# Performance work log

Measured on AMD Instinct MI355X. Metric: run time of the kernel, lower is better.

Reference implementation:

```python
import jax, jax.numpy as jnp
import numpy as np

K_NEIGHBORS = 3  # init kwarg k_neighbors


def setup_inputs() -> dict:
    key = jax.random.key(0)
    k1, k2 = jax.random.split(key)
    q = jax.random.normal(k1, (75, 640, 21, 21), dtype=jnp.float32)
    S = jax.random.normal(k2, (5, 640, 21, 21), dtype=jnp.float32)
    return {"q": q, "S": S, "qAV_num": 1, "SAV_num": 1, "shot_num": 1}


def reference(q, S, qAV_num, SAV_num, shot_num):
    B, C = q.shape[0], q.shape[1]
    # [B, HW, C], L2-normalize each local descriptor over channels
    qd = q.reshape(B, C, -1).transpose(0, 2, 1)
    qd = qd / jnp.linalg.norm(qd, axis=2, keepdims=True)

    N = S.shape[0]
    sd = S.reshape(N, C, -1).transpose(0, 2, 1)  # [N, HW, C]
    sd = sd / jnp.linalg.norm(sd, axis=2, keepdims=True)
    HW = sd.shape[1]
    M = SAV_num * shot_num * HW
    # group support images into classes: [ncls, C, M]
    sup = sd.reshape(-1, M, C).transpose(0, 2, 1)
    ncls = sup.shape[0]

    # cosine similarity: [B, ncls, HW, M]
    ip = jnp.einsum('bqc,ncm->bnqm', qd, sup)
    # split AV groups: [B//qAV, qAV, ncls, HW, M]
    ip = ip.reshape(B // qAV_num, qAV_num, ncls, HW, M)
    # top-k along the query-descriptor (HW) axis (torch dim=-2)
    topk = jax.lax.top_k(jnp.swapaxes(ip, -1, -2), K_NEIGHBORS)[0]  # [..., M, k]
    img2class = topk.sum(axis=(-1, -2))  # [B', qAV, ncls]
    # geometric mean over the AV axis (dim=1)
    sim = jnp.exp(jnp.mean(jnp.log(img2class), axis=1))  # [B', ncls]
    return sim
```

## Files before the change

### kernel.cpp

```cpp
#include <hip/hip_runtime.h>
#include <hip/hip_bf16.h>


#define B_IMGS 75
#define N_CLS  5
#define C_DIM  640
#define HW     441
#define HWP    448
#define NKT    20
#define NRB    28
#define CHUNK  512

typedef __attribute__((ext_vector_type(8))) short  short8;
typedef __attribute__((ext_vector_type(4))) float  float4v;

__device__ __forceinline__ void ins3(float& t0, float& t1, float& t2, float v) {
    float m  = fminf(t0, v);
    t0 = fmaxf(t0, v);
    float m2 = fminf(t1, m);
    t1 = fmaxf(t1, m);
    t2 = fmaxf(t2, m2);
}

__global__ __launch_bounds__(256)
void prep_kernel(const float* __restrict__ q, const float* __restrict__ S,
                 __hip_bfloat16* __restrict__ qn2, __hip_bfloat16* __restrict__ sn2,
                 float* __restrict__ out) {
    __shared__ float part[4][64];
    __shared__ float inv[64];

    int bid = blockIdx.x;
    if (bid == 0) {
        for (int i = threadIdx.x; i < B_IMGS * N_CLS; i += 256) out[i] = 0.f;
    }

    int img = bid / 7;
    int h0  = bid % 7;
    const float* src; __hip_bfloat16* dst;
    if (img < B_IMGS) {
        src = q + (size_t)img * C_DIM * HW;
        dst = qn2 + (size_t)img * NRB * NKT * CHUNK;
    } else {
        src = S + (size_t)(img - B_IMGS) * C_DIM * HW;
        dst = sn2 + (size_t)(img - B_IMGS) * NRB * NKT * CHUNK;
    }
    int t  = threadIdx.x;
    int hl = t & 63;
    int p  = t >> 6;
    int hw = h0 * 64 + hl;
    int hwc = (hw < HW) ? hw : (HW - 1);

    float ss = 0.f;
    for (int c0 = p * 160; c0 < (p + 1) * 160; c0 += 16) {
        float v[16];
#pragma unroll
        for (int j = 0; j < 16; ++j) v[j] = src[(size_t)(c0 + j) * HW + hwc];
#pragma unroll
        for (int j = 0; j < 16; ++j) ss += v[j] * v[j];
    }
    part[p][hl] = ss;
    __syncthreads();
    if (t < 64) {
        float tot = part[0][t] + part[1][t] + part[2][t] + part[3][t];
        inv[t] = (h0 * 64 + t < HW) ? rsqrtf(tot) : 0.f;
    }
    __syncthreads();

    int tl  = hl;
    int row = tl & 15;
    int oct = tl >> 4;
    int rb  = h0 * 4 + p;
    int hw2 = h0 * 64 + p * 16 + row;
    int hw2c = (hw2 < HW) ? hw2 : (HW - 1);
    float iv = inv[p * 16 + row];
    const float* s2 = src + hw2c;
#pragma unroll 2
    for (int kt = 0; kt < NKT; ++kt) {
        float v[8];
#pragma unroll
        for (int j = 0; j < 8; ++j)
            v[j] = s2[(size_t)(kt * 32 + oct * 8 + j) * HW];
        short8 o;
#pragma unroll
        for (int j = 0; j < 8; ++j) {
            __hip_bfloat16 h = __float2bfloat16(v[j] * iv);
            o[j] = *(short*)&h;
        }
        *(short8*)(dst + ((size_t)rb * NKT + kt) * CHUNK + tl * 8) = o;
    }
}

#define LOADA_RB(dstv, r, kt)                                                   \
    dstv = *(const short8*)(pA + ((size_t)((r) * 4 + w) * NKT + (kt)) * CHUNK);

#define LOADB(bS, kt)                                                           \
    {                                                                           \
        _Pragma("unroll")                                                       \
        for (int j = 0; j < 4; ++j)                                             \
            bS[j] = *(const short8*)(pB + ((size_t)j * NKT + (kt)) * CHUNK);    \
    }

__global__ __launch_bounds__(256, 2)
void gemm_top3_kernel(const __hip_bfloat16* __restrict__ qn2,
                      const __hip_bfloat16* __restrict__ sn2,
                      float* __restrict__ out) {
    __shared__ float mrg[4][64][3];

    int id  = blockIdx.x;
    int xcd = id & 7;
    int j8  = id >> 3;
    int b   = (j8 / 35) * 8 + xcd;
    if (b >= B_IMGS) return;
    int inner = j8 % 35;
    int n  = inner / 7;
    int mt = inner % 7;

    int tid  = threadIdx.x;
    int w    = tid >> 6;
    int lane = tid & 63;
    int c16  = lane & 15;
    int quad = lane >> 4;

    const __hip_bfloat16* pA = qn2 + (size_t)b * NRB * NKT * CHUNK + lane * 8;
    const __hip_bfloat16* pB = sn2 + ((size_t)n * NRB + mt * 4) * NKT * CHUNK + lane * 8;

    float4v acc[7][4];
#pragma unroll
    for (int r = 0; r < 7; ++r)
#pragma unroll
        for (int j = 0; j < 4; ++j)
            acc[r][j] = (float4v){0.f, 0.f, 0.f, 0.f};

    short8 as[2][7], bs[2][4];
#pragma unroll
    for (int r = 0; r < 7; ++r) { LOADA_RB(as[0][r], r, 0) }
#pragma unroll
    for (int r = 0; r < 7; ++r) { LOADA_RB(as[1][r], r, 1) }
    LOADB(bs[0], 0)
    LOADB(bs[1], 1)

#pragma unroll
    for (int kt = 0; kt < NKT; ++kt) {
        const int ai = kt & 1;
#pragma unroll
        for (int r = 0; r < 7; ++r) {
            __builtin_amdgcn_s_setprio(1);
#pragma unroll
            for (int j = 0; j < 4; ++j)
                acc[r][j] = __builtin_amdgcn_mfma_f32_16x16x32_bf16(
                    as[ai][r], bs[ai][j], acc[r][j], 0, 0, 0);
            __builtin_amdgcn_s_setprio(0);
            if (kt + 2 < NKT) { LOADA_RB(as[ai][r], r, kt + 2) }
        }
        if (kt + 2 < NKT) LOADB(bs[ai], kt + 2)
    }

    float T0[4], T1[4], T2[4];
#pragma unroll
    for (int j = 0; j < 4; ++j) { T0[j] = -1e30f; T1[j] = -1e30f; T2[j] = -1e30f; }
#pragma unroll
    for (int r = 0; r < 7; ++r)
#pragma unroll
        for (int j = 0; j < 4; ++j)
#pragma unroll
            for (int g = 0; g < 4; ++g) {
                float v = acc[r][j][g];
                if (r == 6) {
                    int row = 384 + w * 16 + quad * 4 + g;
                    if (row >= HW) v = -1e30f;
                }
                ins3(T0[j], T1[j], T2[j], v);
            }

#pragma unroll
    for (int j = 0; j < 4; ++j) {
#pragma unroll
        for (int d = 16; d <= 32; d <<= 1) {
            float o0 = __shfl_xor(T0[j], d, 64);
            float o1 = __shfl_xor(T1[j], d, 64);
            float o2 = __shfl_xor(T2[j], d, 64);
            ins3(T0[j], T1[j], T2[j], o0);
            ins3(T0[j], T1[j], T2[j], o1);
            ins3(T0[j], T1[j], T2[j], o2);
        }
    }

    if (quad == 0) {
#pragma unroll
        for (int j = 0; j < 4; ++j) {
            mrg[w][j * 16 + c16][0] = T0[j];
            mrg[w][j * 16 + c16][1] = T1[j];
            mrg[w][j * 16 + c16][2] = T2[j];
        }
    }
    __syncthreads();
    if (tid < 64) {
        int col = tid;
        float t0 = mrg[0][col][0], t1 = mrg[0][col][1], t2 = mrg[0][col][2];
#pragma unroll
        for (int ww = 1; ww < 4; ++ww) {
            ins3(t0, t1, t2, mrg[ww][col][0]);
            ins3(t0, t1, t2, mrg[ww][col][1]);
            ins3(t0, t1, t2, mrg[ww][col][2]);
        }
        float s = (mt * 64 + col < HW) ? (t0 + t1 + t2) : 0.f;
#pragma unroll
        for (int d = 32; d >= 1; d >>= 1) s += __shfl_xor(s, d, 64);
        if (tid == 0) atomicAdd(&out[b * N_CLS + n], s);
    }
}

extern "C" void kernel_launch(void* const* d_in, const int* in_sizes, int n_in,
                              void* d_out, int out_size, void* d_ws, size_t ws_size,
                              hipStream_t stream) {
    const float* q = (const float*)d_in[0];
    const float* S = (const float*)d_in[1];
    float* out = (float*)d_out;

    char* ws = (char*)d_ws;
    size_t off = 0;
    __hip_bfloat16* qn2 = (__hip_bfloat16*)(ws + off);
    off += (size_t)B_IMGS * NRB * NKT * CHUNK * 2;  off = (off + 255) & ~(size_t)255;
    __hip_bfloat16* sn2 = (__hip_bfloat16*)(ws + off);

    prep_kernel<<<dim3(80 * 7), dim3(256), 0, stream>>>(q, S, qn2, sn2, out);
    gemm_top3_kernel<<<dim3(8 * 350), dim3(256), 0, stream>>>(qn2, sn2, out);
}
```

Measured before the change: 252.8 us.

## Defer L2 normalization to GEMM epilogue, single-pass prep kernel

The prep kernel no longer makes a separate pass over the input to compute per-descriptor norms before converting to bf16. It converts the raw values in one pass, accumulates the sum of squares at the same time, and writes the inverse norms to a small workspace buffer. The GEMM epilogue scales each dot product by the query inverse norm before the top-3 selection and by the support inverse norm after it. This halves global reads in prep at the cost of a few extra loads and multiplies in the epilogue. Storing unnormalized values in bf16 may change rounding slightly.

```diff
diff --git a/kernel.cpp b/kernel.cpp
--- a/kernel.cpp
+++ b/kernel.cpp
@@ -25,10 +25,7 @@
 __global__ __launch_bounds__(256)
 void prep_kernel(const float* __restrict__ q, const float* __restrict__ S,
                  __hip_bfloat16* __restrict__ qn2, __hip_bfloat16* __restrict__ sn2,
-                 float* __restrict__ out) {
-    __shared__ float part[4][64];
-    __shared__ float inv[64];
-
+                 float* __restrict__ invn, float* __restrict__ out) {
     int bid = blockIdx.x;
     if (bid == 0) {
         for (int i = threadIdx.x; i < B_IMGS * N_CLS; i += 256) out[i] = 0.f;
@@ -44,36 +41,17 @@
         src = S + (size_t)(img - B_IMGS) * C_DIM * HW;
         dst = sn2 + (size_t)(img - B_IMGS) * NRB * NKT * CHUNK;
     }
-    int t  = threadIdx.x;
-    int hl = t & 63;
-    int p  = t >> 6;
-    int hw = h0 * 64 + hl;
-    int hwc = (hw < HW) ? hw : (HW - 1);
-
-    float ss = 0.f;
-    for (int c0 = p * 160; c0 < (p + 1) * 160; c0 += 16) {
-        float v[16];
-#pragma unroll
-        for (int j = 0; j < 16; ++j) v[j] = src[(size_t)(c0 + j) * HW + hwc];
-#pragma unroll
-        for (int j = 0; j < 16; ++j) ss += v[j] * v[j];
-    }
-    part[p][hl] = ss;
-    __syncthreads();
-    if (t < 64) {
-        float tot = part[0][t] + part[1][t] + part[2][t] + part[3][t];
-        inv[t] = (h0 * 64 + t < HW) ? rsqrtf(tot) : 0.f;
-    }
-    __syncthreads();
-
-    int tl  = hl;
+    int t   = threadIdx.x;
+    int tl  = t & 63;
+    int p   = t >> 6;
     int row = tl & 15;
     int oct = tl >> 4;
     int rb  = h0 * 4 + p;
     int hw2 = h0 * 64 + p * 16 + row;
-    int hw2c = (hw2 < HW) ? hw2 : (HW - 1);
-    float iv = inv[p * 16 + row];
-    const float* s2 = src + hw2c;
+    int hwc = (hw2 < HW) ? hw2 : (HW - 1);
+    const float* s2 = src + hwc;
+
+    float ss = 0.f;
 #pragma unroll 2
     for (int kt = 0; kt < NKT; ++kt) {
         float v[8];
@@ -83,11 +61,16 @@
         short8 o;
 #pragma unroll
         for (int j = 0; j < 8; ++j) {
-            __hip_bfloat16 h = __float2bfloat16(v[j] * iv);
+            ss += v[j] * v[j];
+            __hip_bfloat16 h = __float2bfloat16(v[j]);
             o[j] = *(short*)&h;
         }
         *(short8*)(dst + ((size_t)rb * NKT + kt) * CHUNK + tl * 8) = o;
     }
+    ss += __shfl_xor(ss, 16, 64);
+    ss += __shfl_xor(ss, 32, 64);
+    if (oct == 0)
+        invn[img * HWP + hw2] = (hw2 < HW) ? rsqrtf(ss) : 0.f;
 }
 
 #define LOADA_RB(dstv, r, kt)                                                   \
@@ -103,6 +86,7 @@
 __global__ __launch_bounds__(256, 2)
 void gemm_top3_kernel(const __hip_bfloat16* __restrict__ qn2,
                       const __hip_bfloat16* __restrict__ sn2,
+                      const float* __restrict__ invn,
                       float* __restrict__ out) {
     __shared__ float mrg[4][64][3];
 
@@ -155,6 +139,11 @@
         if (kt + 2 < NKT) LOADB(bs[ai], kt + 2)
     }
 
+    float4v invr[7];
+#pragma unroll
+    for (int r = 0; r < 7; ++r)
+        invr[r] = *(const float4v*)(invn + (size_t)b * HWP + r * 64 + w * 16 + quad * 4);
+
     float T0[4], T1[4], T2[4];
 #pragma unroll
     for (int j = 0; j < 4; ++j) { T0[j] = -1e30f; T1[j] = -1e30f; T2[j] = -1e30f; }
@@ -164,7 +153,7 @@
         for (int j = 0; j < 4; ++j)
 #pragma unroll
             for (int g = 0; g < 4; ++g) {
-                float v = acc[r][j][g];
+                float v = acc[r][j][g] * invr[r][g];
                 if (r == 6) {
                     int row = 384 + w * 16 + quad * 4 + g;
                     if (row >= HW) v = -1e30f;
@@ -203,7 +192,8 @@
             ins3(t0, t1, t2, mrg[ww][col][1]);
             ins3(t0, t1, t2, mrg[ww][col][2]);
         }
-        float s = (mt * 64 + col < HW) ? (t0 + t1 + t2) : 0.f;
+        float invs_c = invn[(size_t)(B_IMGS + n) * HWP + mt * 64 + col];
+        float s = (mt * 64 + col < HW) ? (t0 + t1 + t2) * invs_c : 0.f;
 #pragma unroll
         for (int d = 32; d >= 1; d >>= 1) s += __shfl_xor(s, d, 64);
         if (tid == 0) atomicAdd(&out[b * N_CLS + n], s);
@@ -222,7 +212,9 @@
     __hip_bfloat16* qn2 = (__hip_bfloat16*)(ws + off);
     off += (size_t)B_IMGS * NRB * NKT * CHUNK * 2;  off = (off + 255) & ~(size_t)255;
     __hip_bfloat16* sn2 = (__hip_bfloat16*)(ws + off);
-
-    prep_kernel<<<dim3(80 * 7), dim3(256), 0, stream>>>(q, S, qn2, sn2, out);
-    gemm_top3_kernel<<<dim3(8 * 350), dim3(256), 0, stream>>>(qn2, sn2, out);
-}
+    off += (size_t)N_CLS * NRB * NKT * CHUNK * 2;   off = (off + 255) & ~(size_t)255;
+    float* invn = (float*)(ws + off);
+
+    prep_kernel<<<dim3(80 * 7), dim3(256), 0, stream>>>(q, S, qn2, sn2, invn, out);
+    gemm_top3_kernel<<<dim3(8 * 350), dim3(256), 0, stream>>>(qn2, sn2, invn, out);
+}
```

After: 240.2 us. -5.0%, faster.
